# Performance work log

Hardware: AMD Instinct MI355X
Metric: run time of the kernel (lower is better)

The kernel has to match this reference:

```python
import jax, jax.numpy as jnp
import numpy as np


def _erode3d(v):
    # torch: -F.max_pool3d(-v, 3, stride=1, padding=1)  == 3x3x3 min-pool, SAME padding
    return -jax.lax.reduce_window(-v, -jnp.inf, jax.lax.max,
                                  (1, 1, 3, 3, 3), (1, 1, 1, 1, 1), 'SAME')


def _chamfer(pred, gt):
    # pred [B,N,3], gt [B,M,3]; squared-euclidean pairwise via |p|^2 + |g|^2 - 2 p.g
    p2 = jnp.sum(pred * pred, axis=-1)            # [B,N]
    g2 = jnp.sum(gt * gt, axis=-1)                # [B,M]
    cross = jnp.einsum('bnd,bmd->bnm', pred, gt)  # [B,N,M]
    d = p2[:, :, None] + g2[:, None, :] - 2.0 * cross
    return jnp.mean(jnp.min(d, axis=2)) + jnp.mean(jnp.min(d, axis=1))


def _cldice(pred_volume, gt_volume, smooth=1e-5):
    pred_skel = _erode3d(jax.nn.sigmoid(pred_volume))
    gt_skel = _erode3d(gt_volume)
    inter = jnp.sum(pred_skel * gt_skel, axis=(2, 3, 4))
    psum = jnp.sum(pred_skel, axis=(2, 3, 4))
    gsum = jnp.sum(gt_skel, axis=(2, 3, 4))
    dice = (2.0 * inter + smooth) / (psum + gsum + smooth)
    return 1.0 - jnp.mean(dice)


def _depth_loss(pred, gt, mask, alpha=0.1, beta=10.0):
    B = pred.shape[0]
    # SILog
    g = (jnp.log(pred + alpha) - jnp.log(gt + alpha)).reshape(B, -1)
    g_mean = jnp.mean(g, axis=1)
    g_var = jnp.mean(g * g, axis=1) - g_mean * g_mean  # biased var
    silog = 10.0 * jnp.mean(g_var) + beta * jnp.mean(g_mean ** 2)
    # gradient L1
    pgx = jnp.abs(pred[:, :-1, :] - pred[:, 1:, :])
    pgy = jnp.abs(pred[:, :, :-1] - pred[:, :, 1:])
    ggx = jnp.abs(gt[:, :-1, :] - gt[:, 1:, :])
    ggy = jnp.abs(gt[:, :, :-1] - gt[:, :, 1:])
    grad_l1 = jnp.mean(jnp.abs(pgx - ggx)) + jnp.mean(jnp.abs(pgy - ggy))
    # masked L1
    mask_l1 = jnp.sum(jnp.abs(pred - gt) * mask) / (jnp.sum(mask) + 1e-8)
    return silog + grad_l1 + mask_l1


def setup_inputs() -> dict:
    key = jax.random.key(0)
    ks = jax.random.split(key, 6)
    B, N, M = 2, 8192, 8192
    D, H, W = 64, 128, 128
    DH, DW = 512, 512
    return {
        'pred_centers': jax.random.normal(ks[0], (B, N, 3), jnp.float32),
        'pred_volume': jax.random.normal(ks[1], (B, 1, D, H, W), jnp.float32),
        'pred_depth': jax.random.uniform(ks[2], (B, DH, DW), jnp.float32),
        'gt_points': jax.random.normal(ks[3], (B, M, 3), jnp.float32),
        'gt_volume': jax.random.uniform(ks[4], (B, 1, D, H, W), jnp.float32),
        'gt_depth': jax.random.uniform(ks[5], (B, DH, DW), jnp.float32),
        'depth_mask': jnp.ones((B, DH, DW), jnp.float32),
        'iteration': 10000,
    }


def reference(pred_centers, pred_volume, pred_depth, gt_points, gt_volume,
              gt_depth, depth_mask, iteration):
    gamma1_base, gamma2, gamma3 = 2.0, 0.5, 0.01
    gamma1 = gamma1_base * np.log(max(int(iteration), 1) / 20000.0)
    chamfer = _chamfer(pred_centers, gt_points)
    cldice = _cldice(pred_volume, gt_volume)
    dloss = _depth_loss(pred_depth, gt_depth, depth_mask)
    total = gamma1 * chamfer + gamma2 * cldice + gamma3 * dloss
    return total
```

## Files before the change

### kernel.cpp

```cpp
#include <hip/hip_runtime.h>
#include <math.h>

#define B 2
#define N 8192
#define M 8192
#define NPTS (B*N)
#define VD 64
#define VH 128
#define VW 128
#define VVOX (VD*VH*VW)
#define DHH 512
#define DWW 512
#define DPIX (DHH*DWW)

#define QT 8
#define SEGS 32
#define TSEG (M/SEGS)

#define OFF_WH_P   0
#define OFF_WH_G   2097152
#define OFF_CHPART 4194304
#define OFF_PCL    5242880
#define OFF_PDE    5244416
#define OFF_PCH    5245952

__device__ __forceinline__ float blockSum(float v, volatile float* sm) {
    #pragma unroll
    for (int o = 32; o > 0; o >>= 1) v += __shfl_down(v, o, 64);
    int lane = threadIdx.x & 63, wid = threadIdx.x >> 6;
    __syncthreads();
    if (lane == 0) sm[wid] = v;
    __syncthreads();
    return sm[0] + sm[1] + sm[2] + sm[3];
}

__device__ __forceinline__ float min3f(float a, float b, float c) {
    return fminf(a, fminf(b, c));
}

__device__ __forceinline__ float sumRange(const float* p, int n, volatile float* sm) {
    float s = 0.f;
    for (int t = threadIdx.x; t < n; t += 256) s += p[t];
    return blockSum(s, sm);
}

__global__ __launch_bounds__(256) void k_phase1(const float* __restrict__ pc,
                                                const float* __restrict__ gp,
                                                const float* __restrict__ pv,
                                                const float* __restrict__ gv,
                                                const float* __restrict__ pd,
                                                const float* __restrict__ gd,
                                                const float* __restrict__ mk,
                                                float* ws) {
    __shared__ float4 smem[TSEG];
    unsigned int bb = blockIdx.x;

    if (bb < 512) {
        int dir  = bb >> 8;
        int rem  = bb & 255;
        int seg  = rem >> 3;
        int qblk = rem & 7;
        const float* Q = dir ? gp : pc;
        const float* T = dir ? pc : gp;
        int qbase = qblk * (256*QT);
        int b = qbase >> 13;

        {
            int t = b*M + seg*TSEG + threadIdx.x;
            float x = T[3*t], y = T[3*t+1], z = T[3*t+2];
            smem[threadIdx.x] = make_float4(x, y, z, x*x + y*y + z*z);
        }
        float nx[QT], ny[QT], nz[QT], q2[QT], dmin[QT];
        #pragma unroll
        for (int k = 0; k < QT; ++k) {
            int i = qbase + k*256 + threadIdx.x;
            float x = Q[3*i], y = Q[3*i+1], z = Q[3*i+2];
            nx[k] = -2.f*x; ny[k] = -2.f*y; nz[k] = -2.f*z;
            q2[k] = x*x + y*y + z*z; dmin[k] = INFINITY;
        }
        __syncthreads();
        #pragma unroll 4
        for (int j = 0; j < TSEG; ++j) {
            float4 tv = smem[j];
            #pragma unroll
            for (int k = 0; k < QT; ++k) {
                float d = fmaf(tv.x, nx[k], fmaf(tv.y, ny[k], fmaf(tv.z, nz[k], tv.w)));
                dmin[k] = fminf(dmin[k], d);
            }
        }
        float* part = ws + OFF_CHPART + dir*(SEGS*NPTS) + seg*NPTS + qbase;
        #pragma unroll
        for (int k = 0; k < QT; ++k)
            part[k*256 + threadIdx.x] = dmin[k] + q2[k];

    } else if (bb < 2560) {
        int r0 = (bb - 512) * 8 + (threadIdx.x >> 5);
        int q  = threadIdx.x & 31;
        int w  = q * 4;
        int b  = r0 >> 13;
        int rb = r0 & 8191;
        int d  = rb >> 7;
        int h  = rb & 127;
        int rowOff = b*VVOX + d*(VH*VW) + h*VW;
        int up = (h > 0)   ? -VW : 0;
        int dn = (h < 127) ?  VW : 0;

        float4 om[2];
        const float* vols[2] = {pv, gv};
        #pragma unroll
        for (int a = 0; a < 2; ++a) {
            const float* row = vols[a] + rowOff;
            float4 acc = make_float4(INFINITY, INFINITY, INFINITY, INFINITY);
            #pragma unroll
            for (int rr = 0; rr < 3; ++rr) {
                const float* rw = row + (rr == 0 ? up : (rr == 2 ? dn : 0));
                float4 c = *(const float4*)(rw + w);
                float l = (q > 0)  ? rw[w-1] : c.x;
                float r = (q < 31) ? rw[w+4] : c.w;
                acc.x = fminf(acc.x, min3f(l,   c.x, c.y));
                acc.y = fminf(acc.y, min3f(c.x, c.y, c.z));
                acc.z = fminf(acc.z, min3f(c.y, c.z, c.w));
                acc.w = fminf(acc.w, min3f(c.z, c.w, r));
            }
            om[a] = acc;
        }
        ((float4*)(ws + OFF_WH_P + rowOff))[q] = om[0];
        ((float4*)(ws + OFF_WH_G + rowOff))[q] = om[1];

    } else {
        volatile float* sm = (volatile float*)smem;
        int idx0 = bb - 2560;
        int b   = idx0 >> 7;
        int blk = idx0 & 127;
        const float* pb = pd + b * DPIX;
        const float* gb = gd + b * DPIX;
        const float* mb = mk + b * DPIX;
        float sg = 0, sg2 = 0, gx = 0, gy = 0, num = 0, den = 0;
        #pragma unroll
        for (int k = 0; k < 8; ++k) {
            int idx = (blk*8 + k)*256 + threadIdx.x;
            int h = idx >> 9;
            int w = idx & 511;
            float p = pb[idx], g = gb[idx], m = mb[idx];
            float lgv = logf(p + 0.1f) - logf(g + 0.1f);
            sg += lgv; sg2 += lgv * lgv;
            if (h < DHH - 1) {
                float p2 = pb[idx + DWW], g2 = gb[idx + DWW];
                gx += fabsf(fabsf(p - p2) - fabsf(g - g2));
            }
            if (w < DWW - 1) {
                float p2 = pb[idx + 1], g2 = gb[idx + 1];
                gy += fabsf(fabsf(p - p2) - fabsf(g - g2));
            }
            num += fabsf(p - g) * m;
            den += m;
        }
        float a;
        float* part = ws + OFF_PDE;
        a = blockSum(sg,  sm); if (threadIdx.x == 0) part[       idx0] = a;
        a = blockSum(sg2, sm); if (threadIdx.x == 0) part[256  + idx0] = a;
        a = blockSum(gx,  sm); if (threadIdx.x == 0) part[512  + idx0] = a;
        a = blockSum(gy,  sm); if (threadIdx.x == 0) part[768  + idx0] = a;
        a = blockSum(num, sm); if (threadIdx.x == 0) part[1024 + idx0] = a;
        a = blockSum(den, sm); if (threadIdx.x == 0) part[1280 + idx0] = a;
    }
}

__global__ __launch_bounds__(256) void k_phase2(float* ws) {
    __shared__ float sm[4];
    unsigned int bb = blockIdx.x;

    if (bb < 64) {
        int dir = bb >> 5;
        int blk = bb & 31;
        const float* base = ws + OFF_CHPART + dir*(SEGS*NPTS) + blk*512;
        float s = 0.f;
        #pragma unroll
        for (int u = 0; u < 2; ++u) {
            int t = u*256 + threadIdx.x;
            float m = INFINITY;
            #pragma unroll
            for (int sg = 0; sg < SEGS; ++sg) m = fminf(m, base[sg*NPTS + t]);
            s += m;
        }
        float a = blockSum(s, sm);
        if (threadIdx.x == 0) ws[OFF_PCH + bb] = a;
    } else {
        int idx0 = bb - 64;
        const float4* whP = (const float4*)(ws + OFF_WH_P);
        const float4* whG = (const float4*)(ws + OFF_WH_G);
        int b   = idx0 >> 8;
        int blk = idx0 & 255;
        float li = 0.f, lp = 0.f, lg = 0.f;
        #pragma unroll
        for (int k = 0; k < 4; ++k) {
            int f4 = b*(VVOX/4) + (blk*4 + k)*256 + threadIdx.x;
            int d  = (f4 >> 12) & 63;
            int up = (d > 0)  ? -4096 : 0;
            int dn = (d < 63) ?  4096 : 0;
            float4 p0 = whP[f4+up], p1 = whP[f4], p2 = whP[f4+dn];
            float4 g0 = whG[f4+up], g1 = whG[f4], g2 = whG[f4+dn];
            float4 mp = make_float4(min3f(p0.x,p1.x,p2.x), min3f(p0.y,p1.y,p2.y),
                                    min3f(p0.z,p1.z,p2.z), min3f(p0.w,p1.w,p2.w));
            float4 mg = make_float4(min3f(g0.x,g1.x,g2.x), min3f(g0.y,g1.y,g2.y),
                                    min3f(g0.z,g1.z,g2.z), min3f(g0.w,g1.w,g2.w));
            float4 ps = make_float4(1.f/(1.f+__expf(-mp.x)), 1.f/(1.f+__expf(-mp.y)),
                                    1.f/(1.f+__expf(-mp.z)), 1.f/(1.f+__expf(-mp.w)));
            li += ps.x*mg.x + ps.y*mg.y + ps.z*mg.z + ps.w*mg.w;
            lp += ps.x + ps.y + ps.z + ps.w;
            lg += mg.x + mg.y + mg.z + mg.w;
        }
        float a;
        float* part = ws + OFF_PCL;
        a = blockSum(li, sm); if (threadIdx.x == 0) part[        idx0] = a;
        a = blockSum(lp, sm); if (threadIdx.x == 0) part[512  + idx0] = a;
        a = blockSum(lg, sm); if (threadIdx.x == 0) part[1024 + idx0] = a;
    }
}

__global__ __launch_bounds__(256) void k_final(const float* ws, const int* iter,
                                               float* out) {
    __shared__ float sm[4];
    float sch = sumRange(ws + OFF_PCH, 64, sm);
    float i0  = sumRange(ws + OFF_PCL,        256, sm);
    float i1  = sumRange(ws + OFF_PCL + 256,  256, sm);
    float p0  = sumRange(ws + OFF_PCL + 512,  256, sm);
    float p1  = sumRange(ws + OFF_PCL + 768,  256, sm);
    float g0  = sumRange(ws + OFF_PCL + 1024, 256, sm);
    float g1  = sumRange(ws + OFF_PCL + 1280, 256, sm);
    float sg0 = sumRange(ws + OFF_PDE,        128, sm);
    float sg1 = sumRange(ws + OFF_PDE + 128,  128, sm);
    float s20 = sumRange(ws + OFF_PDE + 256,  128, sm);
    float s21 = sumRange(ws + OFF_PDE + 384,  128, sm);
    float gx  = sumRange(ws + OFF_PDE + 512,  256, sm);
    float gy  = sumRange(ws + OFF_PDE + 768,  256, sm);
    float num = sumRange(ws + OFF_PDE + 1024, 256, sm);
    float den = sumRange(ws + OFF_PDE + 1280, 256, sm);
    if (threadIdx.x != 0) return;

    float chamfer = sch / (float)NPTS;
    float dsum = (2.f*i0 + 1e-5f) / (p0 + g0 + 1e-5f)
               + (2.f*i1 + 1e-5f) / (p1 + g1 + 1e-5f);
    float cldice = 1.f - 0.5f * dsum;
    float silog = 0.f;
    {
        float gm = sg0 / (float)DPIX;
        float gv = s20 / (float)DPIX - gm*gm;
        silog += 10.f*0.5f*gv + 10.f*0.5f*gm*gm;
        gm = sg1 / (float)DPIX;
        gv = s21 / (float)DPIX - gm*gm;
        silog += 10.f*0.5f*gv + 10.f*0.5f*gm*gm;
    }
    float grad_l1 = gx / (float)(B*(DHH-1)*DWW) + gy / (float)(B*DHH*(DWW-1));
    float mask_l1 = num / (den + 1e-8f);
    float dloss = silog + grad_l1 + mask_l1;
    int it = iter[0]; if (it < 1) it = 1;
    float gamma1 = 2.f * logf((float)it / 20000.f);
    out[0] = gamma1 * chamfer + 0.5f * cldice + 0.01f * dloss;
}

extern "C" void kernel_launch(void* const* d_in, const int* in_sizes, int n_in,
                              void* d_out, int out_size, void* d_ws, size_t ws_size,
                              hipStream_t stream) {
    const float* pc  = (const float*)d_in[0];
    const float* pv  = (const float*)d_in[1];
    const float* pd  = (const float*)d_in[2];
    const float* gp  = (const float*)d_in[3];
    const float* gvv = (const float*)d_in[4];
    const float* gd  = (const float*)d_in[5];
    const float* mk  = (const float*)d_in[6];
    const int*   it  = (const int*)d_in[7];
    float* ws  = (float*)d_ws;
    float* out = (float*)d_out;

    k_phase1<<<2816, 256, 0, stream>>>(pc, gp, pv, gvv, pd, gd, mk, ws);
    k_phase2<<<576,  256, 0, stream>>>(ws);
    k_final <<<1,    256, 0, stream>>>(ws, it, out);
}
```

Measured before the change: 120.0 us.

## Fuse 3D erosion into phase1 with depth sliding window, drop intermediate volumes

The separable min-pool was split across kernels: phase1 wrote W/H-eroded copies of both volumes to workspace, and phase2 re-read three depth planes to finish the erosion and the sums. Now each phase1 block takes 8 depth slices of an 8-row H slab. It keeps a rolling prev/cur/next window of W/H-eroded planes in registers and reduces sigmoid·gt sums directly. This removes the large intermediate write and re-read and shrinks phase2 to the chamfer min only. In exchange it recomputes 2 extra planes per 8 outputs and launches far fewer volume blocks, each doing more serial work, which lowers parallelism.

```diff
diff --git a/kernel.cpp b/kernel.cpp
--- a/kernel.cpp
+++ b/kernel.cpp
@@ -17,12 +17,10 @@
 #define SEGS 32
 #define TSEG (M/SEGS)
 
-#define OFF_WH_P   0
-#define OFF_WH_G   2097152
-#define OFF_CHPART 4194304
-#define OFF_PCL    5242880
-#define OFF_PDE    5244416
-#define OFF_PCH    5245952
+#define OFF_CHPART 0
+#define OFF_PCL    1048576
+#define OFF_PDE    1049344
+#define OFF_PCH    1050880
 
 __device__ __forceinline__ float blockSum(float v, volatile float* sm) {
     #pragma unroll
@@ -42,6 +40,30 @@
     float s = 0.f;
     for (int t = threadIdx.x; t < n; t += 256) s += p[t];
     return blockSum(s, sm);
+}
+
+__device__ __forceinline__ float4 erodeWH(const float* __restrict__ vol,
+                                          int rowU, int rowC, int rowD,
+                                          int w4, int q) {
+    float4 acc = make_float4(INFINITY, INFINITY, INFINITY, INFINITY);
+    int offs[3] = {rowU, rowC, rowD};
+    #pragma unroll
+    for (int r = 0; r < 3; ++r) {
+        const float* rw = vol + offs[r];
+        float4 c = *(const float4*)(rw + w4);
+        float l  = (q > 0)  ? rw[w4-1] : c.x;
+        float rr = (q < 31) ? rw[w4+4] : c.w;
+        acc.x = fminf(acc.x, min3f(l,   c.x, c.y));
+        acc.y = fminf(acc.y, min3f(c.x, c.y, c.z));
+        acc.z = fminf(acc.z, min3f(c.y, c.z, c.w));
+        acc.w = fminf(acc.w, min3f(c.z, c.w, rr));
+    }
+    return acc;
+}
+
+__device__ __forceinline__ float4 min3f4(float4 a, float4 b, float4 c) {
+    return make_float4(min3f(a.x,b.x,c.x), min3f(a.y,b.y,c.y),
+                       min3f(a.z,b.z,c.z), min3f(a.w,b.w,c.w));
 }
 
 __global__ __launch_bounds__(256) void k_phase1(const float* __restrict__ pc,
@@ -93,43 +115,56 @@
         for (int k = 0; k < QT; ++k)
             part[k*256 + threadIdx.x] = dmin[k] + q2[k];
 
-    } else if (bb < 2560) {
-        int r0 = (bb - 512) * 8 + (threadIdx.x >> 5);
-        int q  = threadIdx.x & 31;
-        int w  = q * 4;
-        int b  = r0 >> 13;
-        int rb = r0 & 8191;
-        int d  = rb >> 7;
-        int h  = rb & 127;
-        int rowOff = b*VVOX + d*(VH*VW) + h*VW;
-        int up = (h > 0)   ? -VW : 0;
-        int dn = (h < 127) ?  VW : 0;
-
-        float4 om[2];
-        const float* vols[2] = {pv, gv};
-        #pragma unroll
-        for (int a = 0; a < 2; ++a) {
-            const float* row = vols[a] + rowOff;
-            float4 acc = make_float4(INFINITY, INFINITY, INFINITY, INFINITY);
-            #pragma unroll
-            for (int rr = 0; rr < 3; ++rr) {
-                const float* rw = row + (rr == 0 ? up : (rr == 2 ? dn : 0));
-                float4 c = *(const float4*)(rw + w);
-                float l = (q > 0)  ? rw[w-1] : c.x;
-                float r = (q < 31) ? rw[w+4] : c.w;
-                acc.x = fminf(acc.x, min3f(l,   c.x, c.y));
-                acc.y = fminf(acc.y, min3f(c.x, c.y, c.z));
-                acc.z = fminf(acc.z, min3f(c.y, c.z, c.w));
-                acc.w = fminf(acc.w, min3f(c.z, c.w, r));
-            }
-            om[a] = acc;
-        }
-        ((float4*)(ws + OFF_WH_P + rowOff))[q] = om[0];
-        ((float4*)(ws + OFF_WH_G + rowOff))[q] = om[1];
+    } else if (bb < 768) {
+        volatile float* sm = (volatile float*)smem;
+        int id     = bb - 512;
+        int b      = id >> 7;
+        int rem    = id & 127;
+        int dchunk = rem >> 4;
+        int hslab  = rem & 15;
+        int q      = threadIdx.x & 31;
+        int w4     = q * 4;
+        int h      = hslab*8 + (threadIdx.x >> 5);
+        int d0     = dchunk * 8;
+
+        int base = b*VVOX;
+        int rC = h*VW;
+        int rU = (h > 0)   ? rC - VW : rC;
+        int rD = (h < 127) ? rC + VW : rC;
+
+        int pPrev = base + ((d0 > 0) ? (d0-1) : 0) * (VH*VW);
+        int pCur  = base + d0 * (VH*VW);
+        float4 ppv = erodeWH(pv, pPrev+rU, pPrev+rC, pPrev+rD, w4, q);
+        float4 pgv = erodeWH(gv, pPrev+rU, pPrev+rC, pPrev+rD, w4, q);
+        float4 cpv = erodeWH(pv, pCur+rU,  pCur+rC,  pCur+rD,  w4, q);
+        float4 cgv = erodeWH(gv, pCur+rU,  pCur+rC,  pCur+rD,  w4, q);
+
+        float li = 0.f, lp = 0.f, lg = 0.f;
+        #pragma unroll
+        for (int dd = 0; dd < 8; ++dd) {
+            int d = d0 + dd;
+            int pNext = base + ((d < 63) ? (d+1) : 63) * (VH*VW);
+            float4 npv = erodeWH(pv, pNext+rU, pNext+rC, pNext+rD, w4, q);
+            float4 ngv = erodeWH(gv, pNext+rU, pNext+rC, pNext+rD, w4, q);
+            float4 mp = min3f4(ppv, cpv, npv);
+            float4 mg = min3f4(pgv, cgv, ngv);
+            float4 ps = make_float4(1.f/(1.f+__expf(-mp.x)), 1.f/(1.f+__expf(-mp.y)),
+                                    1.f/(1.f+__expf(-mp.z)), 1.f/(1.f+__expf(-mp.w)));
+            li += ps.x*mg.x + ps.y*mg.y + ps.z*mg.z + ps.w*mg.w;
+            lp += ps.x + ps.y + ps.z + ps.w;
+            lg += mg.x + mg.y + mg.z + mg.w;
+            ppv = cpv; cpv = npv;
+            pgv = cgv; cgv = ngv;
+        }
+        float a;
+        float* part = ws + OFF_PCL;
+        a = blockSum(li, sm); if (threadIdx.x == 0) part[       id] = a;
+        a = blockSum(lp, sm); if (threadIdx.x == 0) part[256  + id] = a;
+        a = blockSum(lg, sm); if (threadIdx.x == 0) part[512  + id] = a;
 
     } else {
         volatile float* sm = (volatile float*)smem;
-        int idx0 = bb - 2560;
+        int idx0 = bb - 768;
         int b   = idx0 >> 7;
         int blk = idx0 & 127;
         const float* pb = pd + b * DPIX;
@@ -169,65 +204,32 @@
 __global__ __launch_bounds__(256) void k_phase2(float* ws) {
     __shared__ float sm[4];
     unsigned int bb = blockIdx.x;
-
-    if (bb < 64) {
-        int dir = bb >> 5;
-        int blk = bb & 31;
-        const float* base = ws + OFF_CHPART + dir*(SEGS*NPTS) + blk*512;
-        float s = 0.f;
-        #pragma unroll
-        for (int u = 0; u < 2; ++u) {
-            int t = u*256 + threadIdx.x;
-            float m = INFINITY;
-            #pragma unroll
-            for (int sg = 0; sg < SEGS; ++sg) m = fminf(m, base[sg*NPTS + t]);
-            s += m;
-        }
-        float a = blockSum(s, sm);
-        if (threadIdx.x == 0) ws[OFF_PCH + bb] = a;
-    } else {
-        int idx0 = bb - 64;
-        const float4* whP = (const float4*)(ws + OFF_WH_P);
-        const float4* whG = (const float4*)(ws + OFF_WH_G);
-        int b   = idx0 >> 8;
-        int blk = idx0 & 255;
-        float li = 0.f, lp = 0.f, lg = 0.f;
-        #pragma unroll
-        for (int k = 0; k < 4; ++k) {
-            int f4 = b*(VVOX/4) + (blk*4 + k)*256 + threadIdx.x;
-            int d  = (f4 >> 12) & 63;
-            int up = (d > 0)  ? -4096 : 0;
-            int dn = (d < 63) ?  4096 : 0;
-            float4 p0 = whP[f4+up], p1 = whP[f4], p2 = whP[f4+dn];
-            float4 g0 = whG[f4+up], g1 = whG[f4], g2 = whG[f4+dn];
-            float4 mp = make_float4(min3f(p0.x,p1.x,p2.x), min3f(p0.y,p1.y,p2.y),
-                                    min3f(p0.z,p1.z,p2.z), min3f(p0.w,p1.w,p2.w));
-            float4 mg = make_float4(min3f(g0.x,g1.x,g2.x), min3f(g0.y,g1.y,g2.y),
-                                    min3f(g0.z,g1.z,g2.z), min3f(g0.w,g1.w,g2.w));
-            float4 ps = make_float4(1.f/(1.f+__expf(-mp.x)), 1.f/(1.f+__expf(-mp.y)),
-                                    1.f/(1.f+__expf(-mp.z)), 1.f/(1.f+__expf(-mp.w)));
-            li += ps.x*mg.x + ps.y*mg.y + ps.z*mg.z + ps.w*mg.w;
-            lp += ps.x + ps.y + ps.z + ps.w;
-            lg += mg.x + mg.y + mg.z + mg.w;
-        }
-        float a;
-        float* part = ws + OFF_PCL;
-        a = blockSum(li, sm); if (threadIdx.x == 0) part[        idx0] = a;
-        a = blockSum(lp, sm); if (threadIdx.x == 0) part[512  + idx0] = a;
-        a = blockSum(lg, sm); if (threadIdx.x == 0) part[1024 + idx0] = a;
-    }
+    int dir = bb >> 5;
+    int blk = bb & 31;
+    const float* base = ws + OFF_CHPART + dir*(SEGS*NPTS) + blk*512;
+    float s = 0.f;
+    #pragma unroll
+    for (int u = 0; u < 2; ++u) {
+        int t = u*256 + threadIdx.x;
+        float m = INFINITY;
+        #pragma unroll
+        for (int sg = 0; sg < SEGS; ++sg) m = fminf(m, base[sg*NPTS + t]);
+        s += m;
+    }
+    float a = blockSum(s, sm);
+    if (threadIdx.x == 0) ws[OFF_PCH + bb] = a;
 }
 
 __global__ __launch_bounds__(256) void k_final(const float* ws, const int* iter,
                                                float* out) {
     __shared__ float sm[4];
     float sch = sumRange(ws + OFF_PCH, 64, sm);
-    float i0  = sumRange(ws + OFF_PCL,        256, sm);
-    float i1  = sumRange(ws + OFF_PCL + 256,  256, sm);
-    float p0  = sumRange(ws + OFF_PCL + 512,  256, sm);
-    float p1  = sumRange(ws + OFF_PCL + 768,  256, sm);
-    float g0  = sumRange(ws + OFF_PCL + 1024, 256, sm);
-    float g1  = sumRange(ws + OFF_PCL + 1280, 256, sm);
+    float i0  = sumRange(ws + OFF_PCL,        128, sm);
+    float i1  = sumRange(ws + OFF_PCL + 128,  128, sm);
+    float p0  = sumRange(ws + OFF_PCL + 256,  128, sm);
+    float p1  = sumRange(ws + OFF_PCL + 384,  128, sm);
+    float g0  = sumRange(ws + OFF_PCL + 512,  128, sm);
+    float g1  = sumRange(ws + OFF_PCL + 640,  128, sm);
     float sg0 = sumRange(ws + OFF_PDE,        128, sm);
     float sg1 = sumRange(ws + OFF_PDE + 128,  128, sm);
     float s20 = sumRange(ws + OFF_PDE + 256,  128, sm);
@@ -273,7 +275,7 @@
     float* ws  = (float*)d_ws;
     float* out = (float*)d_out;
 
-    k_phase1<<<2816, 256, 0, stream>>>(pc, gp, pv, gvv, pd, gd, mk, ws);
-    k_phase2<<<576,  256, 0, stream>>>(ws);
+    k_phase1<<<1024, 256, 0, stream>>>(pc, gp, pv, gvv, pd, gd, mk, ws);
+    k_phase2<<<64,   256, 0, stream>>>(ws);
     k_final <<<1,    256, 0, stream>>>(ws, it, out);
 }
```

New measurement: 158.6 us. 1.32x slower.
